# Performance work log

Measured on AMD Instinct MI355X. Metric: run time of the kernel, lower is better.

Reference implementation:

```python
import jax, jax.numpy as jnp
import numpy as np

DIM = 1024
DEPTH = 8
HEADS = 16
DIM_HEAD = 64
INNER = HEADS * DIM_HEAD  # 1024
NQ = 64
EMB = 768
OUT = 1024
FF_INNER = 4 * DIM
B, N1 = 32, 257
EPS = 1e-5


def layer_norm(x, g, b):
    m = jnp.mean(x, axis=-1, keepdims=True)
    v = jnp.mean(jnp.square(x - m), axis=-1, keepdims=True)
    return (x - m) * jax.lax.rsqrt(v + EPS) * g + b


def split_heads(t):
    # (b, l, inner) -> (b, h, l, dh)
    b, l, _ = t.shape
    return t.reshape(b, l, HEADS, DIM_HEAD).transpose(0, 2, 1, 3)


def setup_inputs() -> dict:
    key = jax.random.key(0)
    ks = jax.random.split(key, 12)
    s = 0.02
    inp = {
        "x": jax.random.normal(ks[0], (B, N1, EMB), jnp.float32),
        "latents": jax.random.normal(ks[1], (1, NQ, DIM), jnp.float32) / np.sqrt(DIM),
        "proj_in_w": jax.random.normal(ks[2], (EMB, DIM), jnp.float32) * s,
        "proj_in_b": jnp.zeros((DIM,), jnp.float32),
        "ln1_g": jnp.ones((DEPTH, DIM), jnp.float32),
        "ln1_b": jnp.zeros((DEPTH, DIM), jnp.float32),
        "ln2_g": jnp.ones((DEPTH, DIM), jnp.float32),
        "ln2_b": jnp.zeros((DEPTH, DIM), jnp.float32),
        "Wq": jax.random.normal(ks[3], (DEPTH, DIM, INNER), jnp.float32) * s,
        "Wkv": jax.random.normal(ks[4], (DEPTH, DIM, 2 * INNER), jnp.float32) * s,
        "Wo": jax.random.normal(ks[5], (DEPTH, INNER, DIM), jnp.float32) * s,
        "ff_ln_g": jnp.ones((DEPTH, DIM), jnp.float32),
        "ff_ln_b": jnp.zeros((DEPTH, DIM), jnp.float32),
        "ff_w1": jax.random.normal(ks[6], (DEPTH, DIM, FF_INNER), jnp.float32) * s,
        "ff_w2": jax.random.normal(ks[7], (DEPTH, FF_INNER, DIM), jnp.float32) * s,
        "proj_out_w": jax.random.uniform(ks[8], (DIM, OUT), jnp.float32, -0.01, 0.01),
        "proj_out_b": jnp.zeros((OUT,), jnp.float32),
        "norm_out_g": jnp.ones((OUT,), jnp.float32),
        "norm_out_b": jnp.zeros((OUT,), jnp.float32),
    }
    return inp


def reference(x, latents, proj_in_w, proj_in_b, ln1_g, ln1_b, ln2_g, ln2_b,
              Wq, Wkv, Wo, ff_ln_g, ff_ln_b, ff_w1, ff_w2,
              proj_out_w, proj_out_b, norm_out_g, norm_out_b):
    # proj_in
    xf = x @ proj_in_w + proj_in_b              # (b, n1, dim)
    lat = jnp.broadcast_to(latents, (x.shape[0], NQ, DIM))
    scale = DIM_HEAD ** -0.25                   # 1/sqrt(sqrt(dim_head))

    for i in range(DEPTH):
        # PerceiverAttention
        xn = layer_norm(xf, ln1_g[i], ln1_b[i])
        ln_lat = layer_norm(lat, ln2_g[i], ln2_b[i])
        q = split_heads(ln_lat @ Wq[i])                       # (b,h,nq,dh)
        kv = jnp.concatenate([xn, ln_lat], axis=1) @ Wkv[i]   # (b,n1+nq,2*inner)
        k, v = jnp.split(kv, 2, axis=-1)
        k, v = split_heads(k), split_heads(v)                 # (b,h,nk,dh)
        w = jnp.einsum('bhqd,bhkd->bhqk', q * scale, k * scale)
        w = jax.nn.softmax(w.astype(jnp.float32), axis=-1).astype(q.dtype)
        o = jnp.einsum('bhqk,bhkd->bhqd', w, v)               # (b,h,nq,dh)
        o = o.transpose(0, 2, 1, 3).reshape(lat.shape[0], NQ, INNER)
        lat = o @ Wo[i] + lat
        # FeedForward: LN -> Linear -> GELU -> Linear
        h = layer_norm(lat, ff_ln_g[i], ff_ln_b[i])
        h = jax.nn.gelu(h @ ff_w1[i], approximate=False) @ ff_w2[i]
        lat = h + lat

    out = lat @ proj_out_w + proj_out_b
    return layer_norm(out, norm_out_g, norm_out_b)
```

## Files before the change

### kernel.cpp

```cpp
#include <hip/hip_runtime.h>
#include <hip/hip_bf16.h>
#include <cstdint>

typedef __hip_bfloat16 bf16;
typedef __attribute__((ext_vector_type(8))) short short8;
typedef __attribute__((ext_vector_type(4))) float f32x4;

__device__ __forceinline__ f32x4 mfma16(short8 a, short8 b, f32x4 c) {
  return __builtin_amdgcn_mfma_f32_16x16x32_bf16(a, b, c, 0, 0, 0);
}

__device__ __forceinline__ void gload16(const bf16* g, bf16* l) {
  __builtin_amdgcn_global_load_lds((const __attribute__((address_space(1))) void*)g,
                                   (__attribute__((address_space(3))) void*)l, 16, 0, 0);
}


__global__ void __launch_bounds__(256) cvt_f32_bf16(const float* __restrict__ in,
                                                    bf16* __restrict__ out, int n4) {
  int i = blockIdx.x * 256 + threadIdx.x;
  if (i < n4) {
    float4 v = *(const float4*)&in[(size_t)i * 4];
    bf16 o[4] = {__float2bfloat16(v.x), __float2bfloat16(v.y),
                 __float2bfloat16(v.z), __float2bfloat16(v.w)};
    *(uint2*)&out[(size_t)i * 4] = *(uint2*)o;
  }
}


__device__ __forceinline__ void trans_tile64(float (*t)[65], const float* __restrict__ src,
                                             bf16* __restrict__ dst, int K, int N,
                                             int bx, int by) {
  int n0 = bx * 64, k0 = by * 64;
  int tx = threadIdx.x & 15, ty = threadIdx.x >> 4;
#pragma unroll
  for (int j = 0; j < 64; j += 16) {
    float4 v = *(const float4*)&src[(size_t)(k0 + ty + j) * N + n0 + tx * 4];
    t[ty + j][tx * 4 + 0] = v.x;
    t[ty + j][tx * 4 + 1] = v.y;
    t[ty + j][tx * 4 + 2] = v.z;
    t[ty + j][tx * 4 + 3] = v.w;
  }
  __syncthreads();
  int cb = tx * 4;
#pragma unroll
  for (int jj = 0; jj < 4; jj++) {
    int r = ty + jj * 16;
    bf16 o[4] = {__float2bfloat16(t[cb + 0][r]), __float2bfloat16(t[cb + 1][r]),
                 __float2bfloat16(t[cb + 2][r]), __float2bfloat16(t[cb + 3][r])};
    *(uint2*)&dst[(size_t)(n0 + r) * K + k0 + cb] = *(uint2*)o;
  }
}

__global__ void __launch_bounds__(256) transpose_cvt(const float* __restrict__ src,
                                                     bf16* __restrict__ dst,
                                                     int K, int N) {
  __shared__ float tile[64][65];
  trans_tile64(tile, src, dst, K, N, blockIdx.x, blockIdx.y);
}

__global__ void __launch_bounds__(256) transpose_all(
    const float* __restrict__ wq, const float* __restrict__ wkv,
    const float* __restrict__ wo, const float* __restrict__ w1,
    const float* __restrict__ w2, bf16* __restrict__ wq_t, bf16* __restrict__ wkv_t,
    bf16* __restrict__ wo_t, bf16* __restrict__ w1_t, bf16* __restrict__ w2_t) {
  __shared__ float tile[64][65];
  int id = blockIdx.x;
  if (id < 256) {
    trans_tile64(tile, wq, wq_t, 1024, 1024, id & 15, id >> 4);
  } else if (id < 768) {
    id -= 256;
    trans_tile64(tile, wkv, wkv_t, 1024, 2048, id & 31, id >> 5);
  } else if (id < 1024) {
    id -= 768;
    trans_tile64(tile, wo, wo_t, 1024, 1024, id & 15, id >> 4);
  } else if (id < 2048) {
    id -= 1024;
    trans_tile64(tile, w1, w1_t, 1024, 4096, id & 63, id >> 6);
  } else {
    id -= 2048;
    trans_tile64(tile, w2, w2_t, 4096, 1024, id & 15, id >> 4);
  }
}


__device__ __forceinline__ void stats4(float4 v, int tid, float& mean,
                                       float& rstd, float* red) {
  float s = v.x + v.y + v.z + v.w;
  float s2 = v.x * v.x + v.y * v.y + v.z * v.z + v.w * v.w;
#pragma unroll
  for (int o = 32; o > 0; o >>= 1) {
    s += __shfl_down(s, o);
    s2 += __shfl_down(s2, o);
  }
  int w = tid >> 6;
  if ((tid & 63) == 0) { red[w] = s; red[4 + w] = s2; }
  __syncthreads();
  s = red[0] + red[1] + red[2] + red[3];
  s2 = red[4] + red[5] + red[6] + red[7];
  mean = s * (1.f / 1024.f);
  float var = s2 * (1.f / 1024.f) - mean * mean;
  rstd = rsqrtf(var + 1e-5f);
}

__device__ __forceinline__ void pack4(bf16* dst, float a, float b, float c, float d) {
  bf16 o[4] = {__float2bfloat16(a), __float2bfloat16(b),
               __float2bfloat16(c), __float2bfloat16(d)};
  *(uint2*)dst = *(uint2*)o;
}

__global__ void __launch_bounds__(256) ln_to_bf16(const float* __restrict__ in,
                                                  const float* __restrict__ g,
                                                  const float* __restrict__ bb,
                                                  bf16* __restrict__ out) {
  __shared__ float red[8];
  int row = blockIdx.x, tid = threadIdx.x, c4 = tid * 4;
  float4 v = *(const float4*)&in[(size_t)row * 1024 + c4];
  float mean, rstd;
  stats4(v, tid, mean, rstd, red);
  float y0 = (v.x - mean) * rstd, y1 = (v.y - mean) * rstd;
  float y2 = (v.z - mean) * rstd, y3 = (v.w - mean) * rstd;
  if (g) {
    float4 gv = *(const float4*)&g[c4];
    float4 bv = *(const float4*)&bb[c4];
    y0 = y0 * gv.x + bv.x; y1 = y1 * gv.y + bv.y;
    y2 = y2 * gv.z + bv.z; y3 = y3 * gv.w + bv.w;
  }
  pack4(&out[(size_t)row * 1024 + c4], y0, y1, y2, y3);
}

template <int LM>
__global__ void __launch_bounds__(256) lncat(const bf16* __restrict__ xhat,
                                             const float* __restrict__ lin,
                                             const float* __restrict__ parts,
                                             const float* __restrict__ lat2,
                                             float* __restrict__ lat,
                                             const float* __restrict__ g1,
                                             const float* __restrict__ b1,
                                             const float* __restrict__ g2,
                                             const float* __restrict__ b2,
                                             bf16* __restrict__ cat,
                                             bf16* __restrict__ lnlat) {
  __shared__ float red[8];
  int row = blockIdx.x, tid = threadIdx.x, c4 = tid * 4;
  int bidx = row / 336, n = row - bidx * 336;
  bf16* out = cat + (size_t)row * 1024;
  const size_t MN = (size_t)2048 * 1024;
  if (n < 257) {
    const bf16* in = xhat + ((size_t)bidx * 257 + n) * 1024;
    uint2 rw = *(const uint2*)&in[c4];
    const bf16* rb = (const bf16*)&rw;
    float4 gv = *(const float4*)&g1[c4];
    float4 bv = *(const float4*)&b1[c4];
    pack4(&out[c4], __bfloat162float(rb[0]) * gv.x + bv.x,
          __bfloat162float(rb[1]) * gv.y + bv.y,
          __bfloat162float(rb[2]) * gv.z + bv.z,
          __bfloat162float(rb[3]) * gv.w + bv.w);
  } else if (n < 321) {
    int lrow = bidx * 64 + (n - 257);
    size_t idx = (size_t)lrow * 1024 + c4;
    float4 a;
    if (LM == 0) {
      a = *(const float4*)&lin[(size_t)(n - 257) * 1024 + c4];
    } else {
      float4 p0 = *(const float4*)&parts[idx];
      float4 p1 = *(const float4*)&parts[MN + idx];
      float4 r2 = *(const float4*)&lat2[idx];
      a.x = p0.x + p1.x + r2.x; a.y = p0.y + p1.y + r2.y;
      a.z = p0.z + p1.z + r2.z; a.w = p0.w + p1.w + r2.w;
    }
    *(float4*)&lat[idx] = a;
    float mean, rstd;
    stats4(a, tid, mean, rstd, red);
    float4 gv = *(const float4*)&g2[c4];
    float4 bv = *(const float4*)&b2[c4];
    bf16 o[4] = {__float2bfloat16((a.x - mean) * rstd * gv.x + bv.x),
                 __float2bfloat16((a.y - mean) * rstd * gv.y + bv.y),
                 __float2bfloat16((a.z - mean) * rstd * gv.z + bv.z),
                 __float2bfloat16((a.w - mean) * rstd * gv.w + bv.w)};
    *(uint2*)&out[c4] = *(uint2*)o;
    *(uint2*)&lnlat[idx] = *(uint2*)o;
  } else {
    uint2 z = {0, 0};
    *(uint2*)&out[c4] = z;
  }
}


enum { MB_BIAS = 1, MB_RESID = 2, MB_GELU = 4, MB_BF16 = 8 };

template <int MODE>
__device__ __forceinline__ void gemm_tile(
    const bf16* __restrict__ A, const bf16* __restrict__ Bt, void* __restrict__ Cout,
    const float* __restrict__ bias, const float* __restrict__ resid,
    int M, int N, int K, int m0, int n0, int kBeg, int kEnd, size_t planeOff,
    bf16* sA, bf16* sB) {
  int tid = threadIdx.x;
  int wave = tid >> 6, lane = tid & 63;
  int quad = lane >> 4, l16 = lane & 15;
  int wm = (wave >> 1) * 64, wn = (wave & 1) * 64;

  int srow = wave * 8 + (lane >> 3);
  int scol = (lane & 7) * 8;
  const bf16* gA[4];
  const bf16* gB[4];
#pragma unroll
  for (int s = 0; s < 4; s++) {
    gA[s] = A + (size_t)min(m0 + s * 32 + srow, M - 1) * K + scol;
    gB[s] = Bt + (size_t)(n0 + s * 32 + srow) * K + scol;
  }
  bf16* lA = &sA[(wave * 8) * 64];
  bf16* lB = &sB[(wave * 8) * 64];

  f32x4 acc[4][4] = {};

  for (int k0 = kBeg; k0 < kEnd; k0 += 64) {
#pragma unroll
    for (int s = 0; s < 4; s++) {
      gload16(gA[s] + k0, lA + s * 32 * 64);
      gload16(gB[s] + k0, lB + s * 32 * 64);
    }
    __syncthreads();
    short8 af[2][4], bfv[2][4];
#pragma unroll
    for (int ks = 0; ks < 2; ks++) {
#pragma unroll
      for (int i = 0; i < 4; i++)
        af[ks][i] = *(const short8*)&sA[(wm + i * 16 + l16) * 64 + ks * 32 + quad * 8];
#pragma unroll
      for (int j = 0; j < 4; j++)
        bfv[ks][j] = *(const short8*)&sB[(wn + j * 16 + l16) * 64 + ks * 32 + quad * 8];
    }
#pragma unroll
    for (int ks = 0; ks < 2; ks++)
#pragma unroll
      for (int i = 0; i < 4; i++)
#pragma unroll
        for (int j = 0; j < 4; j++)
          acc[ks ? i : i][j] = mfma16(af[ks][i], bfv[ks][j], acc[i][j]);
    __syncthreads();
  }

  float* cf = (float*)Cout + planeOff;
#pragma unroll
  for (int i = 0; i < 4; i++) {
    int grb = m0 + wm + i * 16 + quad * 4;
#pragma unroll
    for (int j = 0; j < 4; j++) {
      int gc = n0 + wn + j * 16 + l16;
      float bv = (MODE & MB_BIAS) ? bias[gc] : 0.f;
#pragma unroll
      for (int r = 0; r < 4; r++) {
        int gr = grb + r;
        if (gr < M) {
          float vv = acc[i][j][r] + bv;
          if (MODE & MB_GELU) vv = 0.5f * vv * (1.f + erff(vv * 0.70710678118654752f));
          if (MODE & MB_RESID) vv += resid[(size_t)gr * N + gc];
          if (MODE & MB_BF16) ((bf16*)Cout)[(size_t)gr * N + gc] = __float2bfloat16(vv);
          else cf[(size_t)gr * N + gc] = vv;
        }
      }
    }
  }
}

template <int MODE>
__global__ void __launch_bounds__(256, 2) gemm_bt(
    const bf16* __restrict__ A, const bf16* __restrict__ Bt,
    void* __restrict__ Cout, const float* __restrict__ bias,
    const float* __restrict__ resid, int M, int N, int K) {
  __shared__ bf16 sA[128 * 64];
  __shared__ bf16 sB[128 * 64];
  int kPer = K / gridDim.z;
  gemm_tile<MODE>(A, Bt, Cout, bias, resid, M, N, K,
                  blockIdx.y * 128, blockIdx.x * 128,
                  blockIdx.z * kPer, (blockIdx.z + 1) * kPer,
                  (size_t)blockIdx.z * ((size_t)M * N), sA, sB);
}

__global__ void __launch_bounds__(256, 2) gemm_qkv(
    const bf16* __restrict__ catb, const bf16* __restrict__ wkv,
    bf16* __restrict__ kvbuf, const bf16* __restrict__ lnlat,
    const bf16* __restrict__ wq, bf16* __restrict__ qbuf) {
  __shared__ bf16 sA[128 * 64];
  __shared__ bf16 sB[128 * 64];
  int by = blockIdx.y, bx = blockIdx.x;
  if (by < 84) {
    gemm_tile<MB_BF16>(catb, wkv, kvbuf, nullptr, nullptr, 10752, 2048, 1024,
                       by * 128, bx * 128, 0, 1024, 0, sA, sB);
  } else {
    int t = (by - 84) * 16 + bx;
    gemm_tile<MB_BF16>(lnlat, wq, qbuf, nullptr, nullptr, 2048, 1024, 1024,
                       (t >> 3) * 128, (t & 7) * 128, 0, 1024, 0, sA, sB);
  }
}


enum { RD_BIAS = 1, RD_RESID = 2, RD_BF16 = 4 };

template <int MODE>
__global__ void __launch_bounds__(256) reduce_k(const float* __restrict__ parts, int S,
                                                int MN, int N,
                                                const float* __restrict__ bias,
                                                const float* __restrict__ resid,
                                                void* __restrict__ out) {
  int i4 = (blockIdx.x * 256 + threadIdx.x) * 4;
  if (i4 >= MN) return;
  float4 a = *(const float4*)&parts[i4];
#pragma unroll 4
  for (int s = 1; s < S; s++) {
    float4 b = *(const float4*)&parts[(size_t)s * MN + i4];
    a.x += b.x; a.y += b.y; a.z += b.z; a.w += b.w;
  }
  if (MODE & RD_BIAS) {
    float4 b = *(const float4*)&bias[i4 & (N - 1)];
    a.x += b.x; a.y += b.y; a.z += b.z; a.w += b.w;
  }
  if (MODE & RD_RESID) {
    float4 b = *(const float4*)&resid[i4];
    a.x += b.x; a.y += b.y; a.z += b.z; a.w += b.w;
  }
  if (MODE & RD_BF16) {
    bf16 o[4] = {__float2bfloat16(a.x), __float2bfloat16(a.y),
                 __float2bfloat16(a.z), __float2bfloat16(a.w)};
    *(uint2*)&((bf16*)out)[i4] = *(uint2*)o;
  } else {
    *(float4*)&((float*)out)[i4] = a;
  }
}

__global__ void __launch_bounds__(256) reduce_ln_resid(
    const float* __restrict__ parts, const float* __restrict__ resid,
    const float* __restrict__ g, const float* __restrict__ bb,
    float* __restrict__ lat2, bf16* __restrict__ lnff) {
  __shared__ float red[8];
  int row = blockIdx.x, tid = threadIdx.x, c4 = tid * 4;
  const size_t MN = (size_t)2048 * 1024;
  size_t idx = (size_t)row * 1024 + c4;
  float4 p0 = *(const float4*)&parts[idx];
  float4 p1 = *(const float4*)&parts[MN + idx];
  float4 r2 = *(const float4*)&resid[idx];
  float4 a;
  a.x = p0.x + p1.x + r2.x; a.y = p0.y + p1.y + r2.y;
  a.z = p0.z + p1.z + r2.z; a.w = p0.w + p1.w + r2.w;
  *(float4*)&lat2[idx] = a;
  float mean, rstd;
  stats4(a, tid, mean, rstd, red);
  float4 gv = *(const float4*)&g[c4];
  float4 bv = *(const float4*)&bb[c4];
  pack4(&lnff[idx], (a.x - mean) * rstd * gv.x + bv.x,
        (a.y - mean) * rstd * gv.y + bv.y,
        (a.z - mean) * rstd * gv.z + bv.z,
        (a.w - mean) * rstd * gv.w + bv.w);
}

__global__ void __launch_bounds__(256) reduce_bias_ln(
    const float* __restrict__ parts, const float* __restrict__ bias,
    const float* __restrict__ g, const float* __restrict__ bb,
    float* __restrict__ out) {
  __shared__ float red[8];
  int row = blockIdx.x, tid = threadIdx.x, c4 = tid * 4;
  const size_t MN = (size_t)2048 * 1024;
  size_t idx = (size_t)row * 1024 + c4;
  float4 p0 = *(const float4*)&parts[idx];
  float4 p1 = *(const float4*)&parts[MN + idx];
  float4 bv = *(const float4*)&bias[c4];
  float4 a;
  a.x = p0.x + p1.x + bv.x; a.y = p0.y + p1.y + bv.y;
  a.z = p0.z + p1.z + bv.z; a.w = p0.w + p1.w + bv.w;
  float mean, rstd;
  stats4(a, tid, mean, rstd, red);
  float4 gv = *(const float4*)&g[c4];
  float4 b2 = *(const float4*)&bb[c4];
  float4 o;
  o.x = (a.x - mean) * rstd * gv.x + b2.x;
  o.y = (a.y - mean) * rstd * gv.y + b2.y;
  o.z = (a.z - mean) * rstd * gv.z + b2.z;
  o.w = (a.w - mean) * rstd * gv.w + b2.w;
  *(float4*)&out[idx] = o;
}


__device__ __forceinline__ int swz64(int row, int cb) {
  return (row << 7) + (cb ^ ((row & 7) << 4) ^ (((row >> 3) & 3) << 5));
}

__global__ void __launch_bounds__(256, 2) attn(const bf16* __restrict__ qb,
                                               const bf16* __restrict__ kvb,
                                               bf16* __restrict__ ob) {
  __shared__ bf16 sQ[64 * 64];
  __shared__ bf16 sKV[64 * 64];
  __shared__ bf16 sP[64 * 376];
  __shared__ float sRed[256];
  char* cQ = (char*)sQ;
  char* cKV = (char*)sKV;

  int h = blockIdx.x, b = blockIdx.y;
  int tid = threadIdx.x, wave = tid >> 6, lane = tid & 63;
  int quad = lane >> 4, l16 = lane & 15;

  const bf16* qg = qb + (size_t)b * 64 * 1024 + h * 64;
  const bf16* kg = kvb + (size_t)b * 336 * 2048 + h * 64;
  const bf16* vg = kg + 1024;

  {
    int r = tid >> 3, cb = (tid & 7) * 16;
    *(uint4*)(cQ + swz64(r, cb)) =
        *(const uint4*)((const char*)qg + (size_t)r * 2048 + cb);
    *(uint4*)(cQ + swz64(r + 32, cb)) =
        *(const uint4*)((const char*)qg + (size_t)(r + 32) * 2048 + cb);
  }

  f32x4 accS[6][4] = {};

  for (int g = 0; g < 6; g++) {
    __syncthreads();
    {
      int r = tid >> 3, cb = (tid & 7) * 16;
      int gr = g * 64 + r;
      if (gr < 336)
        *(uint4*)(cKV + swz64(r, cb)) =
            *(const uint4*)((const char*)kg + (size_t)gr * 4096 + cb);
      gr += 32;
      if (gr < 336)
        *(uint4*)(cKV + swz64(r + 32, cb)) =
            *(const uint4*)((const char*)kg + (size_t)gr * 4096 + cb);
    }
    __syncthreads();
    if (g * 4 + wave < 21) {
#pragma unroll
      for (int ks = 0; ks < 2; ks++) {
        short8 bfr = *(const short8*)(cKV + swz64(wave * 16 + l16, ks * 64 + quad * 16));
#pragma unroll
        for (int i = 0; i < 4; i++) {
          short8 afr = *(const short8*)(cQ + swz64(i * 16 + l16, ks * 64 + quad * 16));
          accS[g][i] = mfma16(afr, bfr, accS[g][i]);
        }
      }
    }
  }

  float rmax[4][4], rsum[4][4];
#pragma unroll
  for (int i = 0; i < 4; i++)
#pragma unroll
    for (int r = 0; r < 4; r++) { rmax[i][r] = -1e30f; rsum[i][r] = 0.f; }

#pragma unroll
  for (int g = 0; g < 6; g++) {
    int col = (g * 4 + wave) * 16 + l16;
    bool valid = col < 321;
#pragma unroll
    for (int i = 0; i < 4; i++)
#pragma unroll
      for (int r = 0; r < 4; r++) {
        float v = accS[g][i][r] * 0.125f;
        accS[g][i][r] = v;
        if (valid) rmax[i][r] = fmaxf(rmax[i][r], v);
      }
  }
#pragma unroll
  for (int off = 1; off < 16; off <<= 1)
#pragma unroll
    for (int i = 0; i < 4; i++)
#pragma unroll
      for (int r = 0; r < 4; r++)
        rmax[i][r] = fmaxf(rmax[i][r], __shfl_xor(rmax[i][r], off));
  if (l16 == 0) {
#pragma unroll
    for (int i = 0; i < 4; i++)
#pragma unroll
      for (int r = 0; r < 4; r++)
        sRed[wave * 64 + i * 16 + quad * 4 + r] = rmax[i][r];
  }
  __syncthreads();
#pragma unroll
  for (int i = 0; i < 4; i++)
#pragma unroll
    for (int r = 0; r < 4; r++) {
      int row = i * 16 + quad * 4 + r;
      rmax[i][r] = fmaxf(fmaxf(sRed[row], sRed[64 + row]),
                         fmaxf(sRed[128 + row], sRed[192 + row]));
    }
  __syncthreads();

#pragma unroll
  for (int g = 0; g < 6; g++) {
    int col = (g * 4 + wave) * 16 + l16;
    bool valid = col < 321;
#pragma unroll
    for (int i = 0; i < 4; i++)
#pragma unroll
      for (int r = 0; r < 4; r++) {
        float pv = valid ? __expf(accS[g][i][r] - rmax[i][r]) : 0.f;
        rsum[i][r] += pv;
        if (col < 352) sP[(i * 16 + quad * 4 + r) * 376 + col] = __float2bfloat16(pv);
      }
  }
#pragma unroll
  for (int off = 1; off < 16; off <<= 1)
#pragma unroll
    for (int i = 0; i < 4; i++)
#pragma unroll
      for (int r = 0; r < 4; r++)
        rsum[i][r] += __shfl_xor(rsum[i][r], off);
  if (l16 == 0) {
#pragma unroll
    for (int i = 0; i < 4; i++)
#pragma unroll
      for (int r = 0; r < 4; r++)
        sRed[wave * 64 + i * 16 + quad * 4 + r] = rsum[i][r];
  }
  __syncthreads();
#pragma unroll
  for (int i = 0; i < 4; i++)
#pragma unroll
    for (int r = 0; r < 4; r++) {
      int row = i * 16 + quad * 4 + r;
      rsum[i][r] = sRed[row] + sRed[64 + row] + sRed[128 + row] + sRed[192 + row];
    }

  f32x4 accO[4] = {};
  for (int cch = 0; cch < 6; cch++) {
    __syncthreads();
    {
      int r = tid >> 3, cb = (tid & 7) * 16;
      int gr = cch * 64 + r;
      if (gr < 336)
        *(uint4*)(cKV + swz64(r, cb)) =
            *(const uint4*)((const char*)vg + (size_t)gr * 4096 + cb);
      gr += 32;
      if (gr < 336)
        *(uint4*)(cKV + swz64(r + 32, cb)) =
            *(const uint4*)((const char*)vg + (size_t)gr * 4096 + cb);
    }
    __syncthreads();
    int nks = (cch == 5) ? 1 : 2;
    for (int ks = 0; ks < nks; ks++) {
      short8 bv;
      int cb = (wave * 16 + l16) * 2;
#pragma unroll
      for (int jj = 0; jj < 8; jj++)
        bv[jj] = *(const short*)(cKV + swz64(ks * 32 + quad * 8 + jj, cb));
#pragma unroll
      for (int i = 0; i < 4; i++) {
        short8 ap = *(const short8*)&sP[(i * 16 + l16) * 376 + cch * 64 + ks * 32 + quad * 8];
        accO[i] = mfma16(ap, bv, accO[i]);
      }
    }
  }

#pragma unroll
  for (int i = 0; i < 4; i++)
#pragma unroll
    for (int r = 0; r < 4; r++) {
      int row = i * 16 + quad * 4 + r;
      ob[(size_t)(b * 64 + row) * 1024 + h * 64 + wave * 16 + l16] =
          __float2bfloat16(accO[i][r] / rsum[i][r]);
    }
}


extern "C" void kernel_launch(void* const* d_in, const int* in_sizes, int n_in,
                              void* d_out, int out_size, void* d_ws, size_t ws_size,
                              hipStream_t stream) {
  (void)in_sizes; (void)n_in; (void)out_size; (void)ws_size;
  const float* x    = (const float*)d_in[0];
  const float* lin  = (const float*)d_in[1];
  const float* piw  = (const float*)d_in[2];
  const float* pib  = (const float*)d_in[3];
  const float* ln1g = (const float*)d_in[4];
  const float* ln1b = (const float*)d_in[5];
  const float* ln2g = (const float*)d_in[6];
  const float* ln2b = (const float*)d_in[7];
  const float* Wq   = (const float*)d_in[8];
  const float* Wkv  = (const float*)d_in[9];
  const float* Wo   = (const float*)d_in[10];
  const float* ffg  = (const float*)d_in[11];
  const float* ffb  = (const float*)d_in[12];
  const float* W1   = (const float*)d_in[13];
  const float* W2   = (const float*)d_in[14];
  const float* poW  = (const float*)d_in[15];
  const float* pob  = (const float*)d_in[16];
  const float* nog  = (const float*)d_in[17];
  const float* nob  = (const float*)d_in[18];

  char* p = (char*)d_ws;
  auto alloc = [&](size_t bytes) -> char* {
    char* q = p; p += (bytes + 255) & ~(size_t)255; return q;
  };
  bf16* pin_t  = (bf16*)alloc((size_t)1024 * 768 * 2);
  bf16* pout_t = (bf16*)alloc((size_t)1024 * 1024 * 2);
  bf16* wq_t   = (bf16*)alloc((size_t)1024 * 1024 * 2);
  bf16* wkv_t  = (bf16*)alloc((size_t)2048 * 1024 * 2);
  bf16* wo_t   = (bf16*)alloc((size_t)1024 * 1024 * 2);
  bf16* w1_t   = (bf16*)alloc((size_t)4096 * 1024 * 2);
  bf16* w2_t   = (bf16*)alloc((size_t)1024 * 4096 * 2);
  bf16* x_bf   = (bf16*)alloc((size_t)8224 * 768 * 2);
  float* xf    = (float*)alloc((size_t)8224 * 1024 * 4);
  bf16* xhat   = (bf16*)alloc((size_t)8224 * 1024 * 2);
  bf16* cat    = (bf16*)alloc((size_t)10752 * 1024 * 2);
  bf16* lnlat  = (bf16*)alloc((size_t)2048 * 1024 * 2);
  bf16* qbuf   = (bf16*)alloc((size_t)2048 * 1024 * 2);
  bf16* kvbuf  = (bf16*)alloc((size_t)10752 * 2048 * 2);
  bf16* obuf   = (bf16*)alloc((size_t)2048 * 1024 * 2);
  float* lat   = (float*)alloc((size_t)2048 * 1024 * 4);
  float* lat2  = (float*)alloc((size_t)2048 * 1024 * 4);
  bf16* lnff   = (bf16*)alloc((size_t)2048 * 1024 * 2);
  bf16* h1     = (bf16*)alloc((size_t)2048 * 4096 * 2);

  const int MN = 2048 * 1024;

  cvt_f32_bf16<<<(6316032 / 4 + 255) / 256, 256, 0, stream>>>(x, x_bf, 6316032 / 4);
  transpose_cvt<<<dim3(16, 12), 256, 0, stream>>>(piw, pin_t, 768, 1024);
  transpose_cvt<<<dim3(16, 16), 256, 0, stream>>>(poW, pout_t, 1024, 1024);
  gemm_bt<MB_BIAS><<<dim3(8, 65), 256, 0, stream>>>(x_bf, pin_t, xf, pib, nullptr,
                                                    8224, 1024, 768);
  ln_to_bf16<<<8224, 256, 0, stream>>>(xf, nullptr, nullptr, xhat);

  for (int i = 0; i < 8; i++) {
    transpose_all<<<3072, 256, 0, stream>>>(
        Wq + (size_t)i * 1048576, Wkv + (size_t)i * 2097152, Wo + (size_t)i * 1048576,
        W1 + (size_t)i * 4194304, W2 + (size_t)i * 4194304,
        wq_t, wkv_t, wo_t, w1_t, w2_t);
    if (i == 0)
      lncat<0><<<10752, 256, 0, stream>>>(xhat, lin, nullptr, nullptr, lat,
                                          ln1g + i * 1024, ln1b + i * 1024,
                                          ln2g + i * 1024, ln2b + i * 1024, cat, lnlat);
    else
      lncat<1><<<10752, 256, 0, stream>>>(xhat, nullptr, xf, lat2, lat,
                                          ln1g + i * 1024, ln1b + i * 1024,
                                          ln2g + i * 1024, ln2b + i * 1024, cat, lnlat);
    gemm_qkv<<<dim3(16, 92), 256, 0, stream>>>(cat, wkv_t, kvbuf, lnlat, wq_t, qbuf);
    attn<<<dim3(16, 32), 256, 0, stream>>>(qbuf, kvbuf, obuf);
    gemm_bt<0><<<dim3(8, 16, 2), 256, 0, stream>>>(obuf, wo_t, xf, nullptr, nullptr,
                                                   2048, 1024, 1024);
    reduce_ln_resid<<<2048, 256, 0, stream>>>(xf, lat, ffg + i * 1024, ffb + i * 1024,
                                              lat2, lnff);
    gemm_bt<MB_GELU | MB_BF16><<<dim3(32, 16), 256, 0, stream>>>(lnff, w1_t, h1, nullptr,
                                                                 nullptr, 2048, 4096, 1024);
    gemm_bt<0><<<dim3(8, 16, 2), 256, 0, stream>>>(h1, w2_t, xf, nullptr, nullptr,
                                                   2048, 1024, 4096);
    if (i == 7)
      reduce_k<RD_RESID | RD_BF16><<<MN / 1024, 256, 0, stream>>>(
          xf, 2, MN, 1024, nullptr, lat2, lnff);
  }

  gemm_bt<0><<<dim3(8, 16, 2), 256, 0, stream>>>(lnff, pout_t, xf, nullptr, nullptr,
                                                 2048, 1024, 1024);
  reduce_bias_ln<<<2048, 256, 0, stream>>>(xf, pob, nog, nob, (float*)d_out);
}
```

Baseline: 2.086 ms.

## Halve GEMM K-tile to 32 and raise split-K to four partitions

The shared GEMM tile now stages 32-wide K slices instead of 64, which halves LDS use per block and may allow more resident blocks. The cost is twice as many barriers and loads per unit of K. The Wo, FF2 and proj_out GEMMs now split K four ways, launching 512 blocks instead of 256 to fill the device better. The fused reduce/LayerNorm kernels now sum four partial planes, which adds extra fp32 partial traffic through the xf scratch buffer.

```diff
diff --git a/kernel.cpp b/kernel.cpp
--- a/kernel.cpp
+++ b/kernel.cpp
@@ -165,9 +165,13 @@
     } else {
       float4 p0 = *(const float4*)&parts[idx];
       float4 p1 = *(const float4*)&parts[MN + idx];
+      float4 p2 = *(const float4*)&parts[2 * MN + idx];
+      float4 p3 = *(const float4*)&parts[3 * MN + idx];
       float4 r2 = *(const float4*)&lat2[idx];
-      a.x = p0.x + p1.x + r2.x; a.y = p0.y + p1.y + r2.y;
-      a.z = p0.z + p1.z + r2.z; a.w = p0.w + p1.w + r2.w;
+      a.x = p0.x + p1.x + p2.x + p3.x + r2.x;
+      a.y = p0.y + p1.y + p2.y + p3.y + r2.y;
+      a.z = p0.z + p1.z + p2.z + p3.z + r2.z;
+      a.w = p0.w + p1.w + p2.w + p3.w + r2.w;
     }
     *(float4*)&lat[idx] = a;
     float mean, rstd;
@@ -200,44 +204,37 @@
   int quad = lane >> 4, l16 = lane & 15;
   int wm = (wave >> 1) * 64, wn = (wave & 1) * 64;
 
-  int srow = wave * 8 + (lane >> 3);
-  int scol = (lane & 7) * 8;
-  const bf16* gA[4];
-  const bf16* gB[4];
-#pragma unroll
-  for (int s = 0; s < 4; s++) {
-    gA[s] = A + (size_t)min(m0 + s * 32 + srow, M - 1) * K + scol;
-    gB[s] = Bt + (size_t)(n0 + s * 32 + srow) * K + scol;
-  }
-  bf16* lA = &sA[(wave * 8) * 64];
-  bf16* lB = &sB[(wave * 8) * 64];
+  int srow = wave * 16 + (lane >> 2);
+  int scol = (lane & 3) * 8;
+  const bf16* gA0 = A + (size_t)min(m0 + srow, M - 1) * K + scol;
+  const bf16* gA1 = A + (size_t)min(m0 + 64 + srow, M - 1) * K + scol;
+  const bf16* gB0 = Bt + (size_t)(n0 + srow) * K + scol;
+  const bf16* gB1 = Bt + (size_t)(n0 + 64 + srow) * K + scol;
+  bf16* lA0 = &sA[(wave * 16) * 32];
+  bf16* lA1 = &sA[(64 + wave * 16) * 32];
+  bf16* lB0 = &sB[(wave * 16) * 32];
+  bf16* lB1 = &sB[(64 + wave * 16) * 32];
 
   f32x4 acc[4][4] = {};
 
-  for (int k0 = kBeg; k0 < kEnd; k0 += 64) {
-#pragma unroll
-    for (int s = 0; s < 4; s++) {
-      gload16(gA[s] + k0, lA + s * 32 * 64);
-      gload16(gB[s] + k0, lB + s * 32 * 64);
-    }
+  for (int k0 = kBeg; k0 < kEnd; k0 += 32) {
+    gload16(gA0 + k0, lA0);
+    gload16(gA1 + k0, lA1);
+    gload16(gB0 + k0, lB0);
+    gload16(gB1 + k0, lB1);
     __syncthreads();
-    short8 af[2][4], bfv[2][4];
-#pragma unroll
-    for (int ks = 0; ks < 2; ks++) {
-#pragma unroll
-      for (int i = 0; i < 4; i++)
-        af[ks][i] = *(const short8*)&sA[(wm + i * 16 + l16) * 64 + ks * 32 + quad * 8];
+    short8 af[4], bfv[4];
+#pragma unroll
+    for (int i = 0; i < 4; i++)
+      af[i] = *(const short8*)&sA[(wm + i * 16 + l16) * 32 + quad * 8];
+#pragma unroll
+    for (int j = 0; j < 4; j++)
+      bfv[j] = *(const short8*)&sB[(wn + j * 16 + l16) * 32 + quad * 8];
+#pragma unroll
+    for (int i = 0; i < 4; i++)
 #pragma unroll
       for (int j = 0; j < 4; j++)
-        bfv[ks][j] = *(const short8*)&sB[(wn + j * 16 + l16) * 64 + ks * 32 + quad * 8];
-    }
-#pragma unroll
-    for (int ks = 0; ks < 2; ks++)
-#pragma unroll
-      for (int i = 0; i < 4; i++)
-#pragma unroll
-        for (int j = 0; j < 4; j++)
-          acc[ks ? i : i][j] = mfma16(af[ks][i], bfv[ks][j], acc[i][j]);
+        acc[i][j] = mfma16(af[i], bfv[j], acc[i][j]);
     __syncthreads();
   }
 
@@ -269,8 +266,8 @@
     const bf16* __restrict__ A, const bf16* __restrict__ Bt,
     void* __restrict__ Cout, const float* __restrict__ bias,
     const float* __restrict__ resid, int M, int N, int K) {
-  __shared__ bf16 sA[128 * 64];
-  __shared__ bf16 sB[128 * 64];
+  __shared__ bf16 sA[128 * 32];
+  __shared__ bf16 sB[128 * 32];
   int kPer = K / gridDim.z;
   gemm_tile<MODE>(A, Bt, Cout, bias, resid, M, N, K,
                   blockIdx.y * 128, blockIdx.x * 128,
@@ -282,8 +279,8 @@
     const bf16* __restrict__ catb, const bf16* __restrict__ wkv,
     bf16* __restrict__ kvbuf, const bf16* __restrict__ lnlat,
     const bf16* __restrict__ wq, bf16* __restrict__ qbuf) {
-  __shared__ bf16 sA[128 * 64];
-  __shared__ bf16 sB[128 * 64];
+  __shared__ bf16 sA[128 * 32];
+  __shared__ bf16 sB[128 * 32];
   int by = blockIdx.y, bx = blockIdx.x;
   if (by < 84) {
     gemm_tile<MB_BF16>(catb, wkv, kvbuf, nullptr, nullptr, 10752, 2048, 1024,
@@ -339,10 +336,14 @@
   size_t idx = (size_t)row * 1024 + c4;
   float4 p0 = *(const float4*)&parts[idx];
   float4 p1 = *(const float4*)&parts[MN + idx];
+  float4 p2 = *(const float4*)&parts[2 * MN + idx];
+  float4 p3 = *(const float4*)&parts[3 * MN + idx];
   float4 r2 = *(const float4*)&resid[idx];
   float4 a;
-  a.x = p0.x + p1.x + r2.x; a.y = p0.y + p1.y + r2.y;
-  a.z = p0.z + p1.z + r2.z; a.w = p0.w + p1.w + r2.w;
+  a.x = p0.x + p1.x + p2.x + p3.x + r2.x;
+  a.y = p0.y + p1.y + p2.y + p3.y + r2.y;
+  a.z = p0.z + p1.z + p2.z + p3.z + r2.z;
+  a.w = p0.w + p1.w + p2.w + p3.w + r2.w;
   *(float4*)&lat2[idx] = a;
   float mean, rstd;
   stats4(a, tid, mean, rstd, red);
@@ -364,10 +365,14 @@
   size_t idx = (size_t)row * 1024 + c4;
   float4 p0 = *(const float4*)&parts[idx];
   float4 p1 = *(const float4*)&parts[MN + idx];
+  float4 p2 = *(const float4*)&parts[2 * MN + idx];
+  float4 p3 = *(const float4*)&parts[3 * MN + idx];
   float4 bv = *(const float4*)&bias[c4];
   float4 a;
-  a.x = p0.x + p1.x + bv.x; a.y = p0.y + p1.y + bv.y;
-  a.z = p0.z + p1.z + bv.z; a.w = p0.w + p1.w + bv.w;
+  a.x = p0.x + p1.x + p2.x + p3.x + bv.x;
+  a.y = p0.y + p1.y + p2.y + p3.y + bv.y;
+  a.z = p0.z + p1.z + p2.z + p3.z + bv.z;
+  a.w = p0.w + p1.w + p2.w + p3.w + bv.w;
   float mean, rstd;
   stats4(a, tid, mean, rstd, red);
   float4 gv = *(const float4*)&g[c4];
@@ -633,20 +638,20 @@
                                           ln2g + i * 1024, ln2b + i * 1024, cat, lnlat);
     gemm_qkv<<<dim3(16, 92), 256, 0, stream>>>(cat, wkv_t, kvbuf, lnlat, wq_t, qbuf);
     attn<<<dim3(16, 32), 256, 0, stream>>>(qbuf, kvbuf, obuf);
-    gemm_bt<0><<<dim3(8, 16, 2), 256, 0, stream>>>(obuf, wo_t, xf, nullptr, nullptr,
+    gemm_bt<0><<<dim3(8, 16, 4), 256, 0, stream>>>(obuf, wo_t, xf, nullptr, nullptr,
                                                    2048, 1024, 1024);
     reduce_ln_resid<<<2048, 256, 0, stream>>>(xf, lat, ffg + i * 1024, ffb + i * 1024,
                                               lat2, lnff);
     gemm_bt<MB_GELU | MB_BF16><<<dim3(32, 16), 256, 0, stream>>>(lnff, w1_t, h1, nullptr,
                                                                  nullptr, 2048, 4096, 1024);
-    gemm_bt<0><<<dim3(8, 16, 2), 256, 0, stream>>>(h1, w2_t, xf, nullptr, nullptr,
+    gemm_bt<0><<<dim3(8, 16, 4), 256, 0, stream>>>(h1, w2_t, xf, nullptr, nullptr,
                                                    2048, 1024, 4096);
     if (i == 7)
       reduce_k<RD_RESID | RD_BF16><<<MN / 1024, 256, 0, stream>>>(
-          xf, 2, MN, 1024, nullptr, lat2, lnff);
-  }
-
-  gemm_bt<0><<<dim3(8, 16, 2), 256, 0, stream>>>(lnff, pout_t, xf, nullptr, nullptr,
+          xf, 4, MN, 1024, nullptr, lat2, lnff);
+  }
+
+  gemm_bt<0><<<dim3(8, 16, 4), 256, 0, stream>>>(lnff, pout_t, xf, nullptr, nullptr,
                                                  2048, 1024, 1024);
   reduce_bias_ln<<<2048, 256, 0, stream>>>(xf, pob, nog, nob, (float*)d_out);
 }
```

Measured after the change: 1.991 ms. -4.5%, faster.
